# Performance work log

Hardware: AMD Instinct MI355X
Metric: run time of the kernel (lower is better)

## Reference

```python
import jax, jax.numpy as jnp
import numpy as np


def _make_r2(half_ksize):
    # squared radius grid, shape (K, K, 1, 1) matching TF build()
    coords = jnp.arange(-half_ksize, half_ksize + 1, dtype=jnp.float32)
    x, y = jnp.meshgrid(coords, coords)
    r2 = (x * x + y * y)[:, :, None, None]
    return r2


def setup_inputs() -> dict:
    key = jax.random.key(0)
    k1, k2, k3 = jax.random.split(key, 3)
    half_ksize = 7
    sigma_mean = half_ksize * 0.3 + 0.16  # 2.26, per TruncatedNormal init mean
    x = jax.random.normal(k1, (16, 1024, 1024, 1), dtype=jnp.float32)
    sigma = jnp.float32(sigma_mean) + 0.05 * jax.random.normal(k2, (), dtype=jnp.float32)
    gain = jnp.float32(1.0) + 0.05 * jax.random.normal(k3, (), dtype=jnp.float32)
    return {"x": x, "sigma": sigma, "gain": gain, "half_ksize": half_ksize}


def reference(x, sigma, gain, half_ksize):
    # kernel generation: forward of get_gaussian_circular_kernel_2d
    r2 = _make_r2(half_ksize)                      # (K, K, 1, 1)
    s = jnp.abs(sigma)
    kernel = gain * jnp.exp(-r2 / (2.0 * s * s))   # (K, K, 1, 1) HWIO
    out = jax.lax.conv_general_dilated(
        x, kernel,
        window_strides=(1, 1),
        padding="SAME",
        dimension_numbers=("NHWC", "HWIO", "NHWC"),
    )
    return out
```

## Files before the change

kernel.cpp:

```cpp
#include <hip/hip_runtime.h>
#include <math.h>


#define RAD   7
#define KS    15
#define S     16
#define PRE   (2 * RAD)
#define PADW  8
#define MIDW  (1024 + 2 * PADW)

using f32x4 = __attribute__((ext_vector_type(4))) float;

__global__ __launch_bounds__(256) void gauss_vfirst_kernel(
    const float* __restrict__ x,
    const float* __restrict__ sigma_p,
    const float* __restrict__ gain_p,
    float* __restrict__ out,
    int H, int W)
{
    __shared__ float smid[2][MIDW];

    const int strips = H / S;
    const int n      = blockIdx.x / strips;
    const int strip  = blockIdx.x - n * strips;
    const int row0   = strip * S;

    const int tid = threadIdx.x;
    const int c0  = tid * 4;

    const float* __restrict__ img    = x   + (size_t)n * H * W;
    float*       __restrict__ outimg = out + (size_t)n * H * W;

    const float s    = fabsf(sigma_p[0]);
    const float gain = gain_p[0];
    const float inv  = -1.0f / (2.0f * s * s);
    float w[KS];
#pragma unroll
    for (int j = 0; j < KS; ++j) {
        const float d = (float)(j - RAD);
        w[j] = expf(d * d * inv);
    }

    if (tid < PADW) {
        smid[0][tid] = 0.0f;
        smid[1][tid] = 0.0f;
        smid[0][PADW + 1024 + tid] = 0.0f;
        smid[1][PADW + 1024 + tid] = 0.0f;
    }

    float4 ring[15];
#pragma unroll
    for (int p = 0; p < PRE; ++p) {
        const int gr  = row0 - RAD + p;
        const int grc = max(gr, 0);
        const float m = (gr >= 0) ? 1.0f : 0.0f;
        float4 v = *(const float4*)(img + (size_t)grc * W + c0);
        v.x *= m; v.y *= m; v.z *= m; v.w *= m;
        ring[p] = v;
    }

#pragma unroll
    for (int k = 0; k < S; ++k) {
        {
            const int gr  = row0 + k + RAD;
            const int grc = min(gr, H - 1);
            const float m = (gr < H) ? 1.0f : 0.0f;
            float4 v = *(const float4*)(img + (size_t)grc * W + c0);
            v.x *= m; v.y *= m; v.z *= m; v.w *= m;
            ring[(k + PRE) % 15] = v;
        }

        float4 mid = make_float4(0.f, 0.f, 0.f, 0.f);
#pragma unroll
        for (int i = 0; i < KS; ++i) {
            const float wv  = w[i];
            const float4 r  = ring[(k + i) % 15];
            mid.x += wv * r.x; mid.y += wv * r.y;
            mid.z += wv * r.z; mid.w += wv * r.w;
        }

        const int buf = k & 1;
        *(float4*)&smid[buf][PADW + c0] = mid;
        __syncthreads();

        const float* mp = &smid[buf][c0];
        const float4 f0 = *(const float4*)(mp);
        const float4 f1 = *(const float4*)(mp + 4);
        const float4 f2 = *(const float4*)(mp + 8);
        const float4 f3 = *(const float4*)(mp + 12);
        const float4 f4 = *(const float4*)(mp + 16);
        float f[20] = { f0.x, f0.y, f0.z, f0.w,
                        f1.x, f1.y, f1.z, f1.w,
                        f2.x, f2.y, f2.z, f2.w,
                        f3.x, f3.y, f3.z, f3.w,
                        f4.x, f4.y, f4.z, f4.w };
        float4 acc = make_float4(0.f, 0.f, 0.f, 0.f);
#pragma unroll
        for (int jj = 0; jj < KS; ++jj) {
            const float wv = w[jj];
            acc.x += wv * f[1 + jj];
            acc.y += wv * f[2 + jj];
            acc.z += wv * f[3 + jj];
            acc.w += wv * f[4 + jj];
        }
        acc.x *= gain; acc.y *= gain; acc.z *= gain; acc.w *= gain;

        float* op = outimg + (size_t)(row0 + k) * W + c0;
        __builtin_nontemporal_store(*(const f32x4*)&acc, (f32x4*)op);
    }
}

extern "C" void kernel_launch(void* const* d_in, const int* in_sizes, int n_in,
                              void* d_out, int out_size, void* d_ws, size_t ws_size,
                              hipStream_t stream) {
    const float* x       = (const float*)d_in[0];
    const float* sigma_p = (const float*)d_in[1];
    const float* gain_p  = (const float*)d_in[2];
    float* out = (float*)d_out;

    const int H = 1024, W = 1024;
    const int N = in_sizes[0] / (H * W);

    const dim3 grid(N * (H / S));
    gauss_vfirst_kernel<<<grid, 256, 0, stream>>>(x, sigma_p, gain_p, out, H, W);
}
```

Before: 130.7 us.

## Batch all strip row loads and vertical pass before single barrier

Measured after the change: 130.3 us. Within noise of the previous version (-0.3%).

```diff
diff --git a/kernel.cpp b/kernel.cpp
--- a/kernel.cpp
+++ b/kernel.cpp
@@ -5,20 +5,20 @@
 #define RAD   7
 #define KS    15
 #define S     16
-#define PRE   (2 * RAD)
+#define NIN   (S + 2 * RAD)
 #define PADW  8
 #define MIDW  (1024 + 2 * PADW)
 
 using f32x4 = __attribute__((ext_vector_type(4))) float;
 
-__global__ __launch_bounds__(256) void gauss_vfirst_kernel(
+__global__ __launch_bounds__(256, 2) void gauss_batchv_kernel(
     const float* __restrict__ x,
     const float* __restrict__ sigma_p,
     const float* __restrict__ gain_p,
     float* __restrict__ out,
     int H, int W)
 {
-    __shared__ float smid[2][MIDW];
+    __shared__ float smid[S][MIDW];
 
     const int strips = H / S;
     const int n      = blockIdx.x / strips;
@@ -41,49 +41,51 @@
         w[j] = expf(d * d * inv);
     }
 
-    if (tid < PADW) {
-        smid[0][tid] = 0.0f;
-        smid[1][tid] = 0.0f;
-        smid[0][PADW + 1024 + tid] = 0.0f;
-        smid[1][PADW + 1024 + tid] = 0.0f;
+    {
+        const int o    = tid >> 4;
+        const int pw   = tid & 15;
+        const int word = (pw < 8) ? pw : (1024 + pw);
+        smid[o][word] = 0.0f;
     }
 
-    float4 ring[15];
+    float4 vin[NIN];
 #pragma unroll
-    for (int p = 0; p < PRE; ++p) {
+    for (int p = 0; p < NIN; ++p) {
         const int gr  = row0 - RAD + p;
-        const int grc = max(gr, 0);
-        const float m = (gr >= 0) ? 1.0f : 0.0f;
-        float4 v = *(const float4*)(img + (size_t)grc * W + c0);
+        const int grc = min(max(gr, 0), H - 1);
+        vin[p] = *(const float4*)(img + (size_t)grc * W + c0);
+    }
+
+    float4 acc[S];
+#pragma unroll
+    for (int o = 0; o < S; ++o) acc[o] = make_float4(0.f, 0.f, 0.f, 0.f);
+
+#pragma unroll
+    for (int p = 0; p < NIN; ++p) {
+        const int gr = row0 - RAD + p;
+        const float m = (gr >= 0 && gr < H) ? 1.0f : 0.0f;
+        float4 v = vin[p];
         v.x *= m; v.y *= m; v.z *= m; v.w *= m;
-        ring[p] = v;
+#pragma unroll
+        for (int o = 0; o < S; ++o) {
+            if (o >= p - (KS - 1) && o <= p) {
+                const float wv = w[p - o];
+                acc[o].x += wv * v.x;
+                acc[o].y += wv * v.y;
+                acc[o].z += wv * v.z;
+                acc[o].w += wv * v.w;
+            }
+        }
     }
 
 #pragma unroll
-    for (int k = 0; k < S; ++k) {
-        {
-            const int gr  = row0 + k + RAD;
-            const int grc = min(gr, H - 1);
-            const float m = (gr < H) ? 1.0f : 0.0f;
-            float4 v = *(const float4*)(img + (size_t)grc * W + c0);
-            v.x *= m; v.y *= m; v.z *= m; v.w *= m;
-            ring[(k + PRE) % 15] = v;
-        }
+    for (int o = 0; o < S; ++o)
+        *(float4*)&smid[o][PADW + c0] = acc[o];
+    __syncthreads();
 
-        float4 mid = make_float4(0.f, 0.f, 0.f, 0.f);
 #pragma unroll
-        for (int i = 0; i < KS; ++i) {
-            const float wv  = w[i];
-            const float4 r  = ring[(k + i) % 15];
-            mid.x += wv * r.x; mid.y += wv * r.y;
-            mid.z += wv * r.z; mid.w += wv * r.w;
-        }
-
-        const int buf = k & 1;
-        *(float4*)&smid[buf][PADW + c0] = mid;
-        __syncthreads();
-
-        const float* mp = &smid[buf][c0];
+    for (int o = 0; o < S; ++o) {
+        const float* mp = &smid[o][c0];
         const float4 f0 = *(const float4*)(mp);
         const float4 f1 = *(const float4*)(mp + 4);
         const float4 f2 = *(const float4*)(mp + 8);
@@ -94,19 +96,19 @@
                         f2.x, f2.y, f2.z, f2.w,
                         f3.x, f3.y, f3.z, f3.w,
                         f4.x, f4.y, f4.z, f4.w };
-        float4 acc = make_float4(0.f, 0.f, 0.f, 0.f);
+        float4 a = make_float4(0.f, 0.f, 0.f, 0.f);
 #pragma unroll
         for (int jj = 0; jj < KS; ++jj) {
             const float wv = w[jj];
-            acc.x += wv * f[1 + jj];
-            acc.y += wv * f[2 + jj];
-            acc.z += wv * f[3 + jj];
-            acc.w += wv * f[4 + jj];
+            a.x += wv * f[1 + jj];
+            a.y += wv * f[2 + jj];
+            a.z += wv * f[3 + jj];
+            a.w += wv * f[4 + jj];
         }
-        acc.x *= gain; acc.y *= gain; acc.z *= gain; acc.w *= gain;
+        a.x *= gain; a.y *= gain; a.z *= gain; a.w *= gain;
 
-        float* op = outimg + (size_t)(row0 + k) * W + c0;
-        __builtin_nontemporal_store(*(const f32x4*)&acc, (f32x4*)op);
+        float* op = outimg + (size_t)(row0 + o) * W + c0;
+        __builtin_nontemporal_store(*(const f32x4*)&a, (f32x4*)op);
     }
 }
 
@@ -122,5 +124,5 @@
     const int N = in_sizes[0] / (H * W);
 
     const dim3 grid(N * (H / S));
-    gauss_vfirst_kernel<<<grid, 256, 0, stream>>>(x, sigma_p, gain_p, out, H, W);
+    gauss_batchv_kernel<<<grid, 256, 0, stream>>>(x, sigma_p, gain_p, out, H, W);
 }
```
